# Performance work log

Measured on AMD Instinct MI355X. Metric: run time of the kernel, lower is better.

The kernel has to match this reference:

```python
import jax, jax.numpy as jnp
import numpy as np

WS = 16        # window size
NH = 8         # num heads
EPS = 1e-6
BN_EPS = 1e-5


def _l2norm(t):
    # normalize along the channel (d) axis, which is axis=-2, per position
    return t / jnp.linalg.norm(t, axis=-2, keepdims=True)


def setup_inputs() -> dict:
    key = jax.random.key(0)
    k1, k2, k3 = jax.random.split(key, 3)
    B, C, H, W = 8, 96, 256, 256
    x = jax.random.normal(k1, (B, C, H, W), dtype=jnp.float32)
    w_qkv = jax.random.normal(k2, (3 * C, C), dtype=jnp.float32) * (1.0 / np.sqrt(C))
    w_proj = jax.random.normal(k3, (C, C), dtype=jnp.float32) * (1.0 / np.sqrt(C))
    gamma = jnp.ones((C,), dtype=jnp.float32)
    beta = jnp.zeros((C,), dtype=jnp.float32)
    return {"x": x, "w_qkv": w_qkv, "w_proj": w_proj, "gamma": gamma, "beta": beta}


def reference(x, w_qkv, w_proj, gamma, beta):
    B, C, H, W = x.shape
    ws, nh = WS, NH
    d = C // nh
    # pad H, W up to multiples of ws (static shapes -> jit-safe)
    Hp = (H + ws - 1) // ws * ws
    Wp = (W + ws - 1) // ws * ws
    if (Hp, Wp) != (H, W):
        x = jnp.pad(x, ((0, 0), (0, 0), (0, Hp - H), (0, Wp - W)))
    hh, ww = Hp // ws, Wp // ws

    # 1x1 conv qkv projection (no bias)
    qkv = jnp.einsum('oc,bchw->bohw', w_qkv, x)  # [B, 3C, Hp, Wp]
    # rearrange 'b (qkv h d) (hh ws1) (ww ws2) -> qkv (b hh ww) h d (ws1 ws2)'
    qkv = qkv.reshape(B, 3, nh, d, hh, ws, ww, ws)
    qkv = qkv.transpose(1, 0, 4, 6, 2, 3, 5, 7).reshape(3, B * hh * ww, nh, d, ws * ws)
    q, k, v = qkv[0], qkv[1], qkv[2]  # each [bw, h, d, n]  (n = ws*ws)

    q = _l2norm(q).transpose(0, 1, 3, 2)  # [bw, h, n, d]
    k = _l2norm(k)                        # [bw, h, d, n]

    ksum = k.sum(axis=-1) + EPS           # [bw, h, d]
    tailor = 1.0 / (ws * ws + jnp.einsum('bhnc,bhc->bhn', q, ksum))  # [bw, h, n]

    kv = jnp.einsum('bhmn,bhcn->bhmc', k, v)     # [bw, h, d, d]
    attn = jnp.einsum('bhnm,bhmc->bhcn', q, kv)  # [bw, h, d, n]
    attn = attn + v.sum(axis=-1, keepdims=True)  # broadcast sum_n v over n
    attn = attn * tailor[:, :, None, :]

    # rearrange '(b hh ww) h d (ws1 ws2) -> b (h d) (hh ws1) (ww ws2)'
    out = attn.reshape(B, hh, ww, nh, d, ws, ws)
    out = out.transpose(0, 3, 4, 1, 5, 2, 6).reshape(B, C, Hp, Wp)
    out = out[:, :, :H, :W]

    # proj: 1x1 conv + BatchNorm2d (training-mode batch statistics)
    y = jnp.einsum('oc,bchw->bohw', w_proj, out)
    mean = y.mean(axis=(0, 2, 3), keepdims=True)
    var = y.var(axis=(0, 2, 3), keepdims=True)
    y = (y - mean) * jax.lax.rsqrt(var + BN_EPS)
    y = y * gamma[None, :, None, None] + beta[None, :, None, None]
    return y
```

## Files before the change

### kernel.cpp

```cpp
#include <hip/hip_runtime.h>

typedef short s8v __attribute__((ext_vector_type(8)));
typedef float f4v __attribute__((ext_vector_type(4)));

union F8 { int4 i; s8v s; };
union F8L { long long l[2]; s8v s; };

__device__ __forceinline__ short f2bf(float f){
  union {float f; unsigned u;} v; v.f = f;
  unsigned r = (v.u + 0x7FFFu + ((v.u >> 16) & 1u)) >> 16;
  return (short)r;
}

#define MFMA(a,b,c) __builtin_amdgcn_mfma_f32_16x16x32_bf16((a),(b),(c),0,0,0)

#define WS_W2_OFF   58368
#define WS_ST_OFF   82944
#define N_STAT_SLICES 16
#define WS_OUT_OFF  (1u<<20)

__global__ void prep_kernel(const float* __restrict__ wqkv, const float* __restrict__ wproj,
                            unsigned short* __restrict__ w1, unsigned short* __restrict__ w2p,
                            float* __restrict__ stats){
  int i = blockIdx.x * 256 + threadIdx.x;
  for (int j = i; j < 304*96; j += gridDim.x * 256){
    int row = j / 96, c = j - row * 96;
    float v = (row < 288) ? wqkv[row * 96 + c] : 0.f;
    w1[j] = (unsigned short)f2bf(v);
  }
  for (int j = i; j < 96*128; j += gridDim.x * 256){
    int o = j >> 7, c = j & 127, h = c >> 4, ii = c & 15;
    float v = (ii < 12) ? wproj[o * 96 + h * 12 + ii] : 0.f;
    w2p[j] = (unsigned short)f2bf(v);
  }
  if (i < 192 * N_STAT_SLICES) stats[i] = 0.f;
}

__global__ __launch_bounds__(256,4) void attn_kernel(const float* __restrict__ x,
                                                     const unsigned short* __restrict__ w1,
                                                     short* __restrict__ outp){
  __shared__ short ks[16*264];
  __shared__ short vs[16*264];

  const int tid  = threadIdx.x;
  const int lane = tid & 63, wave = tid >> 6;
  const int quad = lane >> 4, col = lane & 15;
  const int wx = blockIdx.x, wy = blockIdx.y, b = blockIdx.z;
  const int h0 = wy * 16, w0 = wx * 16;

  for (int i = tid; i < 4*264; i += 256){
    int r = 12 + i / 264, cc = i % 264;
    short v = (r == 15) ? (short)0x3F80 : (short)0;
    ks[r*264 + cc] = v; vs[r*264 + cc] = v;
  }

  const float* xb = x + ((size_t)b * 96 << 16);
  s8v Bf[4][3];
  #pragma unroll
  for (int jt = 0; jt < 4; ++jt){
    int t0 = wave * 64 + jt * 16;
    const float* px = xb + (size_t)(h0 + (t0 >> 4)) * 256 + (w0 + col);
    #pragma unroll
    for (int kt = 0; kt < 3; ++kt){
      F8 f;
      #pragma unroll
      for (int j = 0; j < 8; ++j){
        int c = kt * 32 + quad * 8 + j;
        f.s[j] = f2bf(px[(size_t)c << 16]);
      }
      Bf[jt][kt] = f.s;
    }
  }

  for (int h = 0; h < 8; ++h){
    s8v bq[4];
    {
      s8v Aq[3];
      #pragma unroll
      for (int kt = 0; kt < 3; ++kt){
        F8 f; f.i = *(const int4*)(w1 + (h*12 + col) * 96 + kt*32 + quad*8);
        Aq[kt] = f.s;
      }
      #pragma unroll
      for (int jt = 0; jt < 4; ++jt){
        f4v a = {0.f,0.f,0.f,0.f};
        #pragma unroll
        for (int kt = 0; kt < 3; ++kt) a = MFMA(Aq[kt], Bf[jt][kt], a);
        float s = (quad < 3) ? (a[0]*a[0] + a[1]*a[1] + a[2]*a[2] + a[3]*a[3]) : 0.f;
        s += __shfl_xor(s, 16, 64); s += __shfl_xor(s, 32, 64);
        float rq = rsqrtf(s);
        float q0 = a[0]*rq, q1 = a[1]*rq, q2 = a[2]*rq, q3 = a[3]*rq;
        int s0 = (quad == 0) ? col        : (32 + col);
        int s1 = (quad == 0) ? (16 + col) : (32 + col);
        float v0 = __shfl(q0, s0, 64), v1 = __shfl(q1, s0, 64);
        float v2 = __shfl(q2, s0, 64), v3 = __shfl(q3, s0, 64);
        float w4 = __shfl(q0, s1, 64), w5 = __shfl(q1, s1, 64);
        float w6 = __shfl(q2, s1, 64), w7 = __shfl(q3, s1, 64);
        F8 f;
        bool lo = (quad < 2);
        f.s[0] = lo ? f2bf(v0) : (short)0;
        f.s[1] = lo ? f2bf(v1) : (short)0;
        f.s[2] = lo ? f2bf(v2) : (short)0;
        f.s[3] = lo ? f2bf(v3) : (short)0;
        f.s[4] = (quad == 0) ? f2bf(w4) : ((quad == 1) ? (short)0x3F80 : (short)0);
        f.s[5] = (quad == 0) ? f2bf(w5) : (short)0;
        f.s[6] = (quad == 0) ? f2bf(w6) : (short)0;
        f.s[7] = (quad == 0) ? f2bf(w7) : (short)0;
        bq[jt] = f.s;
      }
    }
    __syncthreads();
    {
      s8v Ak[3];
      #pragma unroll
      for (int kt = 0; kt < 3; ++kt){
        F8 f; f.i = *(const int4*)(w1 + (96 + h*12 + col) * 96 + kt*32 + quad*8);
        Ak[kt] = f.s;
      }
      #pragma unroll
      for (int jt = 0; jt < 4; ++jt){
        f4v a = {0.f,0.f,0.f,0.f};
        #pragma unroll
        for (int kt = 0; kt < 3; ++kt) a = MFMA(Ak[kt], Bf[jt][kt], a);
        float s = (quad < 3) ? (a[0]*a[0] + a[1]*a[1] + a[2]*a[2] + a[3]*a[3]) : 0.f;
        s += __shfl_xor(s, 16, 64); s += __shfl_xor(s, 32, 64);
        float rk = rsqrtf(s);
        if (quad < 3){
          int t = wave*64 + jt*16 + col;
          #pragma unroll
          for (int r = 0; r < 4; ++r) ks[(quad*4 + r)*264 + t] = f2bf(a[r]*rk);
        }
      }
    }
    {
      s8v Av[3];
      #pragma unroll
      for (int kt = 0; kt < 3; ++kt){
        F8 f; f.i = *(const int4*)(w1 + (192 + h*12 + col) * 96 + kt*32 + quad*8);
        Av[kt] = f.s;
      }
      #pragma unroll
      for (int jt = 0; jt < 4; ++jt){
        f4v a = {0.f,0.f,0.f,0.f};
        #pragma unroll
        for (int kt = 0; kt < 3; ++kt) a = MFMA(Av[kt], Bf[jt][kt], a);
        if (quad < 3){
          int t = wave*64 + jt*16 + col;
          #pragma unroll
          for (int r = 0; r < 4; ++r) vs[(quad*4 + r)*264 + t] = f2bf(a[r]);
        }
      }
    }
    __syncthreads();

    f4v kvv = {0.f,0.f,0.f,0.f};
    #pragma unroll
    for (int kk = 0; kk < 8; ++kk){
      F8 a, bv;
      a.i  = *(const int4*)&ks[col*264 + kk*32 + quad*8];
      bv.i = *(const int4*)&vs[col*264 + kk*32 + quad*8];
      kvv = MFMA(a.s, bv.s, kvv);
    }
    F8 fa;
    {
      int cc = (col == 12) ? 15 : col;
      int l0 = ((quad << 1) << 4) | cc;
      int l1 = (((quad << 1) + 1) << 4) | cc;
      float v;
      v = __shfl(kvv[0], l0 & 63, 64); fa.s[0] = f2bf((quad < 2) ? v : 0.f);
      v = __shfl(kvv[1], l0 & 63, 64); fa.s[1] = f2bf((quad < 2) ? v : 0.f);
      v = __shfl(kvv[2], l0 & 63, 64); fa.s[2] = f2bf((quad < 2) ? v : 0.f);
      v = __shfl(kvv[3], l0 & 63, 64); fa.s[3] = f2bf((quad < 2) ? v : 0.f);
      float v0  = __shfl(kvv[0], l1 & 63, 64);
      float v15 = __shfl(kvv[3], 48 | cc, 64);
      fa.s[4] = f2bf((quad == 0) ? v0 : ((quad == 1) ? v15 : 0.f));
      v = __shfl(kvv[1], l1 & 63, 64); fa.s[5] = f2bf((quad == 0) ? v : 0.f);
      v = __shfl(kvv[2], l1 & 63, 64); fa.s[6] = f2bf((quad == 0) ? v : 0.f);
      v = __shfl(kvv[3], l1 & 63, 64); fa.s[7] = f2bf((quad == 0) ? v : 0.f);
    }
    #pragma unroll
    for (int jt = 0; jt < 4; ++jt){
      int t0 = wave*64 + jt*16;
      f4v z = {0.f,0.f,0.f,0.f};
      f4v d2 = MFMA(fa.s, bq[jt], z);
      float dot = __shfl(d2[0], 48 + col, 64);
      float tl = 1.f / dot;
      if (quad < 3){
        int pix = (h0 + (t0 >> 4)) * 256 + (w0 + col);
        short* po = outp + ((size_t)((b*8 + h) * 65536 + pix)) * 12 + quad*4;
        short4 pk; pk.x = f2bf(d2[0]*tl); pk.y = f2bf(d2[1]*tl); pk.z = f2bf(d2[2]*tl); pk.w = f2bf(d2[3]*tl);
        *(short4*)po = pk;
      }
    }
  }
}

__device__ __forceinline__ void load_proj_bfrag(const short* __restrict__ outp,
                                                int b, int pixrow, int wave, int quad, int col,
                                                s8v Bf[4][4]){
  #pragma unroll
  for (int jt = 0; jt < 4; ++jt){
    int pix = pixrow + wave*64 + jt*16 + col;
    #pragma unroll
    for (int kt = 0; kt < 4; ++kt){
      int h = kt*2 + (quad >> 1);
      const short* pb = outp + ((size_t)((b*8 + h) * 65536 + pix)) * 12;
      F8L f;
      if ((quad & 1) == 0){ f.l[0] = *(const long long*)(pb);     f.l[1] = *(const long long*)(pb + 4); }
      else                { f.l[0] = *(const long long*)(pb + 8); f.l[1] = 0; }
      Bf[jt][kt] = f.s;
    }
  }
}

__global__ __launch_bounds__(256,4) void projy32_kernel(const short* __restrict__ outp,
                                                        const unsigned short* __restrict__ w2p,
                                                        float* __restrict__ stats,
                                                        float* __restrict__ y){
  __shared__ float sld[192];
  const int tid = threadIdx.x;
  if (tid < 192) sld[tid] = 0.f;
  __syncthreads();
  const int lane = tid & 63, wave = tid >> 6;
  const int quad = lane >> 4, col = lane & 15;
  const int hrow = blockIdx.x, b = blockIdx.y;

  s8v Bf[4][4];
  load_proj_bfrag(outp, b, hrow*256, wave, quad, col, Bf);

  float* yb = y + ((size_t)(b*96) << 16) + (size_t)hrow * 256;

  #pragma unroll
  for (int mt = 0; mt < 6; ++mt){
    s8v Af[4];
    #pragma unroll
    for (int kt = 0; kt < 4; ++kt){
      F8 f; f.i = *(const int4*)(w2p + (mt*16 + col)*128 + kt*32 + quad*8);
      Af[kt] = f.s;
    }
    float rs[4] = {0.f,0.f,0.f,0.f}, rss[4] = {0.f,0.f,0.f,0.f};
    #pragma unroll
    for (int jt = 0; jt < 4; ++jt){
      int n0 = wave*64 + jt*16;
      f4v a = {0.f,0.f,0.f,0.f};
      #pragma unroll
      for (int kt = 0; kt < 4; ++kt) a = MFMA(Af[kt], Bf[jt][kt], a);
      #pragma unroll
      for (int r = 0; r < 4; ++r){
        float v = a[r]; rs[r] += v; rss[r] += v*v;
        int ch = mt*16 + quad*4 + r;
        yb[((size_t)ch << 16) + n0 + col] = v;
      }
    }
    #pragma unroll
    for (int r = 0; r < 4; ++r){
      float a1 = rs[r], a2 = rss[r];
      a1 += __shfl_xor(a1, 1, 64); a2 += __shfl_xor(a2, 1, 64);
      a1 += __shfl_xor(a1, 2, 64); a2 += __shfl_xor(a2, 2, 64);
      a1 += __shfl_xor(a1, 4, 64); a2 += __shfl_xor(a2, 4, 64);
      a1 += __shfl_xor(a1, 8, 64); a2 += __shfl_xor(a2, 8, 64);
      if (col == 0){
        int o = mt*16 + quad*4 + r;
        atomicAdd(&sld[o], a1);
        atomicAdd(&sld[96 + o], a2);
      }
    }
  }
  __syncthreads();
  if (tid < 192) atomicAdd(&stats[(blockIdx.x & (N_STAT_SLICES-1))*192 + tid], sld[tid]);
}

__global__ __launch_bounds__(256,8) void bnfix_kernel(const float* __restrict__ stats,
                                                      const float* __restrict__ gamma,
                                                      const float* __restrict__ beta,
                                                      float* __restrict__ y){
  __shared__ float sc[96], sh[96];
  const int tid = threadIdx.x;
  if (tid < 96){
    float s1 = 0.f, s2 = 0.f;
    #pragma unroll
    for (int s = 0; s < N_STAT_SLICES; ++s){ s1 += stats[s*192 + tid]; s2 += stats[s*192 + 96 + tid]; }
    const float invN = 1.f / 524288.f;
    float m  = s1 * invN;
    float var = s2 * invN - m*m;
    float s = gamma[tid] * rsqrtf(var + 1e-5f);
    sc[tid] = s; sh[tid] = beta[tid] - m * s;
  }
  __syncthreads();

  const long long ngroups = (8LL*96*65536) / 8;
  for (long long g = (long long)blockIdx.x * 256 + tid; g < ngroups; g += (long long)gridDim.x * 256){
    long long base = g * 8;
    int ch = (int)((base >> 16) % 96);
    float scc = sc[ch], shh = sh[ch];
    f4v v0 = *(f4v*)(y + base);
    f4v v1 = *(f4v*)(y + base + 4);
    #pragma unroll
    for (int j = 0; j < 4; ++j){ v0[j] = v0[j]*scc + shh; v1[j] = v1[j]*scc + shh; }
    *(f4v*)(y + base) = v0;
    *(f4v*)(y + base + 4) = v1;
  }
}

extern "C" void kernel_launch(void* const* d_in, const int* in_sizes, int n_in,
                              void* d_out, int out_size, void* d_ws, size_t ws_size,
                              hipStream_t stream){
  const float* x     = (const float*)d_in[0];
  const float* wqkv  = (const float*)d_in[1];
  const float* wproj = (const float*)d_in[2];
  const float* gamma = (const float*)d_in[3];
  const float* beta  = (const float*)d_in[4];
  char* ws = (char*)d_ws;
  unsigned short* w1  = (unsigned short*)(ws);
  unsigned short* w2p = (unsigned short*)(ws + WS_W2_OFF);
  float* stats = (float*)(ws + WS_ST_OFF);
  short* outp  = (short*)(ws + WS_OUT_OFF);
  float* y = (float*)d_out;

  hipLaunchKernelGGL(prep_kernel, dim3(64), dim3(256), 0, stream, wqkv, wproj, w1, w2p, stats);
  hipLaunchKernelGGL(attn_kernel, dim3(16, 16, 8), dim3(256), 0, stream, x, w1, outp);
  hipLaunchKernelGGL(projy32_kernel, dim3(256, 8), dim3(256), 0, stream, outp, w2p, stats, y);
  hipLaunchKernelGGL(bnfix_kernel, dim3(2048), dim3(256), 0, stream, stats, gamma, beta, y);
}
```

Baseline: 561.2 us.

## Fuse windowed attention with output projection and drop intermediate buffer

Merges the attention kernel and the projection/statistics kernel so that each window's per-head attention output is shuffled in registers into MFMA B-fragments and projected immediately. This removes the bf16 intermediate round trip through global memory and one kernel launch. The BN fix-up kernel is also re-indexed to a 2D grid with a per-row channel, which avoids the 64-bit modulo per group. In exchange, register pressure rises (launch bounds drop to 3 blocks per CU, with an unrolled head loop holding bpair fragments), and y writes become 16-wide strided per window row.

```diff
diff --git a/kernel.cpp b/kernel.cpp
--- a/kernel.cpp
+++ b/kernel.cpp
@@ -4,7 +4,6 @@
 typedef float f4v __attribute__((ext_vector_type(4)));
 
 union F8 { int4 i; s8v s; };
-union F8L { long long l[2]; s8v s; };
 
 __device__ __forceinline__ short f2bf(float f){
   union {float f; unsigned u;} v; v.f = f;
@@ -17,7 +16,6 @@
 #define WS_W2_OFF   58368
 #define WS_ST_OFF   82944
 #define N_STAT_SLICES 16
-#define WS_OUT_OFF  (1u<<20)
 
 __global__ void prep_kernel(const float* __restrict__ wqkv, const float* __restrict__ wproj,
                             unsigned short* __restrict__ w1, unsigned short* __restrict__ w2p,
@@ -36,11 +34,14 @@
   if (i < 192 * N_STAT_SLICES) stats[i] = 0.f;
 }
 
-__global__ __launch_bounds__(256,4) void attn_kernel(const float* __restrict__ x,
-                                                     const unsigned short* __restrict__ w1,
-                                                     short* __restrict__ outp){
+__global__ __launch_bounds__(256,3) void attnproj_kernel(const float* __restrict__ x,
+                                                         const unsigned short* __restrict__ w1,
+                                                         const unsigned short* __restrict__ w2p,
+                                                         float* __restrict__ stats,
+                                                         float* __restrict__ y){
   __shared__ short ks[16*264];
   __shared__ short vs[16*264];
+  __shared__ float sld[192];
 
   const int tid  = threadIdx.x;
   const int lane = tid & 63, wave = tid >> 6;
@@ -48,6 +49,8 @@
   const int wx = blockIdx.x, wy = blockIdx.y, b = blockIdx.z;
   const int h0 = wy * 16, w0 = wx * 16;
 
+  if (tid < 192) sld[tid] = 0.f;
+
   for (int i = tid; i < 4*264; i += 256){
     int r = 12 + i / 264, cc = i % 264;
     short v = (r == 15) ? (short)0x3F80 : (short)0;
@@ -72,6 +75,9 @@
     }
   }
 
+  s8v bpair[4][4];
+
+  #pragma unroll
   for (int h = 0; h < 8; ++h){
     s8v bq[4];
     {
@@ -180,56 +186,27 @@
     }
     #pragma unroll
     for (int jt = 0; jt < 4; ++jt){
-      int t0 = wave*64 + jt*16;
       f4v z = {0.f,0.f,0.f,0.f};
       f4v d2 = MFMA(fa.s, bq[jt], z);
       float dot = __shfl(d2[0], 48 + col, 64);
       float tl = 1.f / dot;
-      if (quad < 3){
-        int pix = (h0 + (t0 >> 4)) * 256 + (w0 + col);
-        short* po = outp + ((size_t)((b*8 + h) * 65536 + pix)) * 12 + quad*4;
-        short4 pk; pk.x = f2bf(d2[0]*tl); pk.y = f2bf(d2[1]*tl); pk.z = f2bf(d2[2]*tl); pk.w = f2bf(d2[3]*tl);
-        *(short4*)po = pk;
-      }
-    }
-  }
-}
-
-__device__ __forceinline__ void load_proj_bfrag(const short* __restrict__ outp,
-                                                int b, int pixrow, int wave, int quad, int col,
-                                                s8v Bf[4][4]){
-  #pragma unroll
-  for (int jt = 0; jt < 4; ++jt){
-    int pix = pixrow + wave*64 + jt*16 + col;
-    #pragma unroll
-    for (int kt = 0; kt < 4; ++kt){
-      int h = kt*2 + (quad >> 1);
-      const short* pb = outp + ((size_t)((b*8 + h) * 65536 + pix)) * 12;
-      F8L f;
-      if ((quad & 1) == 0){ f.l[0] = *(const long long*)(pb);     f.l[1] = *(const long long*)(pb + 4); }
-      else                { f.l[0] = *(const long long*)(pb + 8); f.l[1] = 0; }
-      Bf[jt][kt] = f.s;
-    }
-  }
-}
-
-__global__ __launch_bounds__(256,4) void projy32_kernel(const short* __restrict__ outp,
-                                                        const unsigned short* __restrict__ w2p,
-                                                        float* __restrict__ stats,
-                                                        float* __restrict__ y){
-  __shared__ float sld[192];
-  const int tid = threadIdx.x;
-  if (tid < 192) sld[tid] = 0.f;
-  __syncthreads();
-  const int lane = tid & 63, wave = tid >> 6;
-  const int quad = lane >> 4, col = lane & 15;
-  const int hrow = blockIdx.x, b = blockIdx.y;
-
-  s8v Bf[4][4];
-  load_proj_bfrag(outp, b, hrow*256, wave, quad, col, Bf);
-
-  float* yb = y + ((size_t)(b*96) << 16) + (size_t)hrow * 256;
-
+      float o0 = d2[0]*tl, o1 = d2[1]*tl, o2 = d2[2]*tl, o3 = d2[3]*tl;
+      int sj0 = ((quad & 1) == 0) ? col        : (32 + col);
+      int sj1 = ((quad & 1) == 0) ? (16 + col) : (32 + col);
+      F8 fb;
+      fb.s[0] = f2bf(__shfl(o0, sj0, 64));
+      fb.s[1] = f2bf(__shfl(o1, sj0, 64));
+      fb.s[2] = f2bf(__shfl(o2, sj0, 64));
+      fb.s[3] = f2bf(__shfl(o3, sj0, 64));
+      fb.s[4] = f2bf(__shfl(o0, sj1, 64));
+      fb.s[5] = f2bf(__shfl(o1, sj1, 64));
+      fb.s[6] = f2bf(__shfl(o2, sj1, 64));
+      fb.s[7] = f2bf(__shfl(o3, sj1, 64));
+      if ((quad >> 1) == (h & 1)) bpair[h >> 1][jt] = fb.s;
+    }
+  }
+
+  float* yb = y + ((size_t)(b*96) << 16);
   #pragma unroll
   for (int mt = 0; mt < 6; ++mt){
     s8v Af[4];
@@ -241,15 +218,15 @@
     float rs[4] = {0.f,0.f,0.f,0.f}, rss[4] = {0.f,0.f,0.f,0.f};
     #pragma unroll
     for (int jt = 0; jt < 4; ++jt){
-      int n0 = wave*64 + jt*16;
       f4v a = {0.f,0.f,0.f,0.f};
       #pragma unroll
-      for (int kt = 0; kt < 4; ++kt) a = MFMA(Af[kt], Bf[jt][kt], a);
+      for (int kt = 0; kt < 4; ++kt) a = MFMA(Af[kt], bpair[kt][jt], a);
+      int pix = (h0 + wave*4 + jt) * 256 + (w0 + col);
       #pragma unroll
       for (int r = 0; r < 4; ++r){
         float v = a[r]; rs[r] += v; rss[r] += v*v;
         int ch = mt*16 + quad*4 + r;
-        yb[((size_t)ch << 16) + n0 + col] = v;
+        yb[((size_t)ch << 16) + pix] = v;
       }
     }
     #pragma unroll
@@ -288,17 +265,16 @@
   }
   __syncthreads();
 
-  const long long ngroups = (8LL*96*65536) / 8;
-  for (long long g = (long long)blockIdx.x * 256 + tid; g < ngroups; g += (long long)gridDim.x * 256){
-    long long base = g * 8;
-    int ch = (int)((base >> 16) % 96);
-    float scc = sc[ch], shh = sh[ch];
-    f4v v0 = *(f4v*)(y + base);
-    f4v v1 = *(f4v*)(y + base + 4);
-    #pragma unroll
-    for (int j = 0; j < 4; ++j){ v0[j] = v0[j]*scc + shh; v1[j] = v1[j]*scc + shh; }
-    *(f4v*)(y + base) = v0;
-    *(f4v*)(y + base + 4) = v1;
+  const int row = blockIdx.y;
+  const int ch  = row % 96;
+  const float scc = sc[ch], shh = sh[ch];
+  float* p = y + ((size_t)row << 16) + blockIdx.x * 8192;
+  #pragma unroll
+  for (int i = 0; i < 8; ++i){
+    f4v v = *(f4v*)(p + (i*256 + tid)*4);
+    #pragma unroll
+    for (int j = 0; j < 4; ++j) v[j] = v[j]*scc + shh;
+    *(f4v*)(p + (i*256 + tid)*4) = v;
   }
 }
 
@@ -314,11 +290,9 @@
   unsigned short* w1  = (unsigned short*)(ws);
   unsigned short* w2p = (unsigned short*)(ws + WS_W2_OFF);
   float* stats = (float*)(ws + WS_ST_OFF);
-  short* outp  = (short*)(ws + WS_OUT_OFF);
   float* y = (float*)d_out;
 
   hipLaunchKernelGGL(prep_kernel, dim3(64), dim3(256), 0, stream, wqkv, wproj, w1, w2p, stats);
-  hipLaunchKernelGGL(attn_kernel, dim3(16, 16, 8), dim3(256), 0, stream, x, w1, outp);
-  hipLaunchKernelGGL(projy32_kernel, dim3(256, 8), dim3(256), 0, stream, outp, w2p, stats, y);
-  hipLaunchKernelGGL(bnfix_kernel, dim3(2048), dim3(256), 0, stream, stats, gamma, beta, y);
-}
+  hipLaunchKernelGGL(attnproj_kernel, dim3(16, 16, 8), dim3(256), 0, stream, x, w1, w2p, stats, y);
+  hipLaunchKernelGGL(bnfix_kernel, dim3(8, 768), dim3(256), 0, stream, stats, gamma, beta, y);
+}
```

New measurement: 572.7 us. 2.0% more time.
